# Kernel optimization log

Measured on AMD Instinct MI355X. Metric: run time of the kernel, lower is better.

## Reference

```python
import jax, jax.numpy as jnp
import numpy as np

EPS = 1e-8


def setup_inputs() -> dict:
    key = jax.random.key(0)
    ks = jax.random.split(key, 6)
    B, Cin, Cout, K, S, G = 8, 64, 64, 3, 512, 48
    fan_in = Cin * K * K * K
    bound_w = np.sqrt(6.0 / ((1 + 0.25 ** 2) * fan_in))  # kaiming_uniform a=0.25
    bound_b = 1.0 / np.sqrt(fan_in)
    bound_lin = 1.0 / np.sqrt(S)
    return {
        "x": jax.random.normal(ks[0], (B, Cin, G, G, G), jnp.float32),
        "style": jax.random.normal(ks[1], (B, S), jnp.float32),
        "weight": jax.random.uniform(ks[2], (Cout, Cin, K, K, K), jnp.float32, -bound_w, bound_w),
        "bias": jax.random.uniform(ks[3], (1, Cout, 1, 1, 1), jnp.float32, -bound_b, bound_b),
        "style_w": jax.random.uniform(ks[4], (Cin, S), jnp.float32, -bound_lin, bound_lin),
        "style_b": jax.random.uniform(ks[5], (Cin,), jnp.float32, -bound_lin, bound_lin),
    }


def reference(x, style, weight, bias, style_w, style_b):
    B, Cin = x.shape[0], x.shape[1]
    Cout, K = weight.shape[0], weight.shape[2]
    # style modulation scale per (sample, input channel)
    s = style @ style_w.T + style_b                      # [B, Cin]
    # modulate: per-sample weights [B, Cout, Cin, K, K, K]
    w = weight[None] * s[:, None, :, None, None, None]
    # demodulate: rsqrt of per-(sample, out-channel) variance
    var = jnp.sum(w * w, axis=(2, 3, 4, 5), keepdims=True)
    w = w * jax.lax.rsqrt(var + EPS)
    # grouped conv: merge batch into channels, groups = batch_size
    w = w.reshape(B * Cout, Cin, K, K, K)
    xg = x.reshape(1, B * Cin, *x.shape[2:])
    y = jax.lax.conv_general_dilated(
        xg, w,
        window_strides=(1, 1, 1),
        padding='VALID',
        dimension_numbers=('NCDHW', 'OIDHW', 'NCDHW'),
        feature_group_count=B,
    )
    y = y.reshape(B, Cout, *y.shape[2:])
    return y + bias
```

## Files before the change

### kernel.cpp

```cpp
#include <hip/hip_runtime.h>


typedef __bf16 bf16x8 __attribute__((ext_vector_type(8)));
typedef float  f32x4  __attribute__((ext_vector_type(4)));

static constexpr int   B_   = 8;
static constexpr int   S_   = 512;
static constexpr int   G_   = 48;
static constexpr int   O_   = 46;
static constexpr int   TAPS = 27;
static constexpr int   SPI  = G_ * G_ * G_;
static constexpr int   SPO  = O_ * O_ * O_;
static constexpr float EPSV = 1e-8f;

static constexpr size_t XT_OFF   = 0;
static constexpr size_t XT_BYTES = (size_t)B_ * SPI * 64 * 2;
static constexpr size_t WQ_OFF   = XT_OFF + XT_BYTES;
static constexpr size_t WQ_BYTES = (size_t)B_ * 2 * TAPS * 64 * 32 * 2;
static constexpr size_t S_OFF    = WQ_OFF + WQ_BYTES;
static constexpr size_t D_OFF    = S_OFF + 2048;

__device__ __forceinline__ unsigned short f2bf(float f) {
    unsigned int u = __float_as_uint(f);
    u = (u + 0x7fffu + ((u >> 16) & 1u)) >> 16;
    return (unsigned short)u;
}

__global__ void s_kernel(const float* __restrict__ style,
                         const float* __restrict__ style_w,
                         const float* __restrict__ style_b,
                         float* __restrict__ s_out)
{
    const int bg = blockIdx.x, b = bg >> 6, g = bg & 63, l = threadIdx.x;
    const float4* sp = (const float4*)(style + b * S_);
    const float4* wp = (const float4*)(style_w + g * S_);
    const float4 a0 = sp[l * 2], a1 = sp[l * 2 + 1];
    const float4 b0 = wp[l * 2], b1 = wp[l * 2 + 1];
    float acc = a0.x * b0.x + a0.y * b0.y + a0.z * b0.z + a0.w * b0.w
              + a1.x * b1.x + a1.y * b1.y + a1.z * b1.z + a1.w * b1.w;
#pragma unroll
    for (int m = 1; m <= 32; m <<= 1) acc += __shfl_xor(acc, m);
    if (l == 0) s_out[bg] = acc + style_b[g];
}

__global__ void d_kernel(const float* __restrict__ weight,
                         const float* __restrict__ s,
                         float* __restrict__ d_out)
{
    const int bc = blockIdx.x, b = bc >> 6, co = bc & 63, ci = threadIdx.x;
    const float sv = s[b * 64 + ci];
    const float* wp = weight + (co * 64 + ci) * TAPS;
    float v = 0.f;
#pragma unroll
    for (int i = 0; i < TAPS; ++i) { const float t = wp[i] * sv; v += t * t; }
#pragma unroll
    for (int m = 1; m <= 32; m <<= 1) v += __shfl_xor(v, m);
    if (ci == 0) d_out[bc] = rsqrtf(v + EPSV);
}

__global__ void wq_kernel(const float* __restrict__ weight,
                          const float* __restrict__ s,
                          const float* __restrict__ d,
                          unsigned short* __restrict__ wq)
{
    const int blk = blockIdx.x;
    const int b = blk / 27, tap = blk - b * 27;
    const int t = threadIdx.x;
#pragma unroll
    for (int it = 0; it < 2; ++it) {
        const int item = t + it * 256;
        const int kc = item >> 8;
        const int g  = (item >> 6) & 3;
        const int l  = item & 63;
        const int co = g * 16 + (l & 15);
        const int ci0 = kc * 32 + ((l >> 4) * 8);
        const float dd = d[b * 64 + co];
        unsigned int u[4];
#pragma unroll
        for (int k = 0; k < 4; ++k) {
            const int ci = ci0 + 2 * k;
            const float w0 = weight[(co * 64 + ci)     * TAPS + tap] * s[b * 64 + ci]     * dd;
            const float w1 = weight[(co * 64 + ci + 1) * TAPS + tap] * s[b * 64 + ci + 1] * dd;
            u[k] = (unsigned)f2bf(w0) | ((unsigned)f2bf(w1) << 16);
        }
        uint4 v; v.x = u[0]; v.y = u[1]; v.z = u[2]; v.w = u[3];
        *(uint4*)(wq + ((size_t)((b * 2 + kc) * 27 + tap)) * 2048 + (g * 64 + l) * 8) = v;
    }
}

__global__ void xT_kernel(const float* __restrict__ x,
                          unsigned short* __restrict__ xT)
{
    const int blk = blockIdx.x;
    const int b = blk / 1728;
    const int sp0 = (blk - b * 1728) * 64;
    const int t = threadIdx.x;
    __shared__ float tile[64][65];

    const int spl = t & 63;
    const int c4 = t >> 6;
#pragma unroll
    for (int p = 0; p < 16; ++p) {
        const int ci = c4 * 16 + p;
        tile[ci][spl] = x[((size_t)b * 64 + ci) * SPI + sp0 + spl];
    }
    __syncthreads();

    const int ci8 = (t & 7) * 8;
    const int spq = t >> 3;
#pragma unroll
    for (int p = 0; p < 2; ++p) {
        const int sp = spq + 32 * p;
        unsigned int u[4];
#pragma unroll
        for (int k = 0; k < 4; ++k) {
            const unsigned int lo = f2bf(tile[ci8 + 2 * k][sp]);
            const unsigned int hi = f2bf(tile[ci8 + 2 * k + 1][sp]);
            u[k] = lo | (hi << 16);
        }
        uint4 v; v.x = u[0]; v.y = u[1]; v.z = u[2]; v.w = u[3];
        *(uint4*)(xT + ((size_t)b * SPI + sp0 + sp) * 64 + ci8) = v;
    }
}

#define XST     80
#define XTILE_B (648 * 80)

__global__ __launch_bounds__(256, 3) void conv_kernel(
    const unsigned short* __restrict__ xT,
    const unsigned short* __restrict__ wq,
    const float* __restrict__ bias,
    float* __restrict__ out)
{
    __shared__ __align__(16) char xs[XTILE_B];

    const int t = threadIdx.x;
    const int p  = blockIdx.x;
    const int lg = (p & 7) * 432 + (p >> 3);
    const int xt = lg % 3;
    const int r0 = lg / 3;
    const int yt = r0 % 12;
    const int bz = r0 / 12;
    const int b  = bz / 12, zt = bz - b * 12;
    const int x0 = xt * 16;
    const int y0 = (yt < 11) ? yt * 4 : 42;
    const int z0 = (zt < 11) ? zt * 4 : 42;

    const unsigned short* const xb = xT + (size_t)b * (SPI * 64);
    const unsigned short* const wb = wq + (size_t)b * (2 * TAPS * 2048);

    const int w = t >> 6, l = t & 63, kg = l >> 4, l16 = l & 15;
    const int bbase = (w * 108 + l16) * XST + kg * 16;

    f32x4 acc[16];
#pragma unroll
    for (int i = 0; i < 16; ++i) acc[i] = (f32x4){0.f, 0.f, 0.f, 0.f};

#pragma unroll 1
    for (int kc = 0; kc < 2; ++kc) {
        const unsigned short* const wkc = wb + (size_t)kc * (TAPS * 2048);

        if (kc) __syncthreads();

        for (int i = t; i < 2592; i += 256) {
            const int sp = i >> 2, cg = i & 3;
            const int iz = sp / 108;
            const int r1 = sp - iz * 108;
            const int iy = r1 / 18;
            const int ix = r1 - iy * 18;
            int gx = x0 + ix; if (gx > 47) gx = 47;
            const uint4 v = *(const uint4*)(xb +
                ((((z0 + iz) * 48) + (y0 + iy)) * 48 + gx) * 64 + kc * 32 + cg * 8);
            *(uint4*)(xs + sp * XST + cg * 16) = v;
        }

        bf16x8 a[4];
#pragma unroll
        for (int g = 0; g < 4; ++g)
            a[g] = *(const bf16x8*)(wkc + g * 512 + l * 8);

        __syncthreads();

#pragma unroll 1
        for (int tap = 0; tap < TAPS; ++tap) {
            const int tnx = (tap + 1 < TAPS) ? tap + 1 : tap;
            bf16x8 an[4];
#pragma unroll
            for (int g = 0; g < 4; ++g)
                an[g] = *(const bf16x8*)(wkc + (size_t)tnx * 2048 + g * 512 + l * 8);

            const int kz = tap / 9;
            const int r2 = tap - kz * 9;
            const int ky = r2 / 3;
            const int kx = r2 - ky * 3;
            const int toff = ((kz * 6 + ky) * 18 + kx) * XST;

            bf16x8 b0 = *(const bf16x8*)(xs + toff + bbase);
            bf16x8 b1 = *(const bf16x8*)(xs + toff + bbase + 18 * XST);
            bf16x8 b2 = *(const bf16x8*)(xs + toff + bbase + 36 * XST);
            bf16x8 b3 = *(const bf16x8*)(xs + toff + bbase + 54 * XST);

            acc[0]  = __builtin_amdgcn_mfma_f32_16x16x32_bf16(a[0], b0, acc[0],  0, 0, 0);
            acc[1]  = __builtin_amdgcn_mfma_f32_16x16x32_bf16(a[0], b1, acc[1],  0, 0, 0);
            acc[2]  = __builtin_amdgcn_mfma_f32_16x16x32_bf16(a[0], b2, acc[2],  0, 0, 0);
            acc[3]  = __builtin_amdgcn_mfma_f32_16x16x32_bf16(a[0], b3, acc[3],  0, 0, 0);
            acc[4]  = __builtin_amdgcn_mfma_f32_16x16x32_bf16(a[1], b0, acc[4],  0, 0, 0);
            acc[5]  = __builtin_amdgcn_mfma_f32_16x16x32_bf16(a[1], b1, acc[5],  0, 0, 0);
            acc[6]  = __builtin_amdgcn_mfma_f32_16x16x32_bf16(a[1], b2, acc[6],  0, 0, 0);
            acc[7]  = __builtin_amdgcn_mfma_f32_16x16x32_bf16(a[1], b3, acc[7],  0, 0, 0);
            acc[8]  = __builtin_amdgcn_mfma_f32_16x16x32_bf16(a[2], b0, acc[8],  0, 0, 0);
            acc[9]  = __builtin_amdgcn_mfma_f32_16x16x32_bf16(a[2], b1, acc[9],  0, 0, 0);
            acc[10] = __builtin_amdgcn_mfma_f32_16x16x32_bf16(a[2], b2, acc[10], 0, 0, 0);
            acc[11] = __builtin_amdgcn_mfma_f32_16x16x32_bf16(a[2], b3, acc[11], 0, 0, 0);
            acc[12] = __builtin_amdgcn_mfma_f32_16x16x32_bf16(a[3], b0, acc[12], 0, 0, 0);
            acc[13] = __builtin_amdgcn_mfma_f32_16x16x32_bf16(a[3], b1, acc[13], 0, 0, 0);
            acc[14] = __builtin_amdgcn_mfma_f32_16x16x32_bf16(a[3], b2, acc[14], 0, 0, 0);
            acc[15] = __builtin_amdgcn_mfma_f32_16x16x32_bf16(a[3], b3, acc[15], 0, 0, 0);

#pragma unroll
            for (int g = 0; g < 4; ++g) a[g] = an[g];
        }
    }

    const size_t ob = (size_t)b * 64 * SPO;
    const int oz = z0 + w;
    const int ox = x0 + l16;
    const bool xok = (ox < O_);
    if (xok) {
#pragma unroll
        for (int g = 0; g < 4; ++g) {
#pragma unroll
            for (int nt = 0; nt < 4; ++nt) {
                const int oy = y0 + nt;
                const f32x4 v = acc[g * 4 + nt];
                const size_t so = (size_t)oz * 2116 + oy * 46 + ox;
#pragma unroll
                for (int r = 0; r < 4; ++r) {
                    const int co = g * 16 + kg * 4 + r;
                    out[ob + (size_t)co * SPO + so] = v[r] + bias[co];
                }
            }
        }
    }
}

extern "C" void kernel_launch(void* const* d_in, const int* in_sizes, int n_in,
                              void* d_out, int out_size, void* d_ws, size_t ws_size,
                              hipStream_t stream)
{
    const float* x       = (const float*)d_in[0];
    const float* style   = (const float*)d_in[1];
    const float* weight  = (const float*)d_in[2];
    const float* bias    = (const float*)d_in[3];
    const float* style_w = (const float*)d_in[4];
    const float* style_b = (const float*)d_in[5];
    float* out = (float*)d_out;

    char* ws = (char*)d_ws;
    unsigned short* xT  = (unsigned short*)(ws + XT_OFF);
    unsigned short* wqp = (unsigned short*)(ws + WQ_OFF);
    float* sbuf = (float*)(ws + S_OFF);
    float* dbuf = (float*)(ws + D_OFF);

    hipLaunchKernelGGL(s_kernel, dim3(512), dim3(64), 0, stream,
                       style, style_w, style_b, sbuf);
    hipLaunchKernelGGL(d_kernel, dim3(512), dim3(64), 0, stream,
                       weight, sbuf, dbuf);
    hipLaunchKernelGGL(wq_kernel, dim3(216), dim3(256), 0, stream,
                       weight, sbuf, dbuf, wqp);
    hipLaunchKernelGGL(xT_kernel, dim3(B_ * (SPI / 64)), dim3(256), 0, stream,
                       x, xT);
    hipLaunchKernelGGL(conv_kernel, dim3(3456), dim3(256), 0, stream,
                       xT, wqp, bias, out);
}
```

Baseline: 588.9 us.

## Prefetch second channel chunk into registers and remap warps to 2x8 output tiles

```diff
diff --git a/kernel.cpp b/kernel.cpp
--- a/kernel.cpp
+++ b/kernel.cpp
@@ -97,12 +97,16 @@
     const int t = threadIdx.x;
     __shared__ float tile[64][65];
 
-    const int spl = t & 63;
-    const int c4 = t >> 6;
-#pragma unroll
-    for (int p = 0; p < 16; ++p) {
-        const int ci = c4 * 16 + p;
-        tile[ci][spl] = x[((size_t)b * 64 + ci) * SPI + sp0 + spl];
+    const int cr = t >> 4;
+    const int s4 = (t & 15) * 4;
+#pragma unroll
+    for (int r = 0; r < 4; ++r) {
+        const int ci = r * 16 + cr;
+        const float4 v = *(const float4*)(x + ((size_t)b * 64 + ci) * SPI + sp0 + s4);
+        tile[ci][s4]     = v.x;
+        tile[ci][s4 + 1] = v.y;
+        tile[ci][s4 + 2] = v.z;
+        tile[ci][s4 + 3] = v.w;
     }
     __syncthreads();
 
@@ -150,93 +154,101 @@
     const unsigned short* const wb = wq + (size_t)b * (2 * TAPS * 2048);
 
     const int w = t >> 6, l = t & 63, kg = l >> 4, l16 = l & 15;
-    const int bbase = (w * 108 + l16) * XST + kg * 16;
+    const int ch = w & 1, zp = w >> 1;
+    const unsigned short* const wa = wb + ch * 1024 + l * 8;
+    const int bbase = (zp * 216 + l16) * XST + kg * 16;
+    constexpr int FOFF[8] = {0, 1440, 2880, 4320, 8640, 10080, 11520, 12960};
 
     f32x4 acc[16];
 #pragma unroll
     for (int i = 0; i < 16; ++i) acc[i] = (f32x4){0.f, 0.f, 0.f, 0.f};
 
+    auto x_src = [&](int i, int kc) -> const uint4* {
+        const int sp = i >> 2, cg = i & 3;
+        const int iz = sp / 108;
+        const int r1 = sp - iz * 108;
+        const int iy = r1 / 18;
+        const int ix = r1 - iy * 18;
+        int gx = x0 + ix; if (gx > 47) gx = 47;
+        return (const uint4*)(xb +
+            ((((z0 + iz) * 48) + (y0 + iy)) * 48 + gx) * 64 + kc * 32 + cg * 8);
+    };
+
+#pragma unroll
+    for (int j = 0; j < 10; ++j) {
+        const int i = t + j * 256;
+        const uint4 v = *x_src(i, 0);
+        *(uint4*)(xs + (i >> 2) * XST + (i & 3) * 16) = v;
+    }
+    if (t < 32) {
+        const int i = 2560 + t;
+        const uint4 v = *x_src(i, 0);
+        *(uint4*)(xs + (i >> 2) * XST + (i & 3) * 16) = v;
+    }
+
+    bf16x8 a0 = *(const bf16x8*)(wa);
+    bf16x8 a1 = *(const bf16x8*)(wa + 512);
+
+    __syncthreads();
+
+    uint4 pv[10];
+#pragma unroll
+    for (int j = 0; j < 10; ++j)
+        pv[j] = *x_src(t + j * 256, 1);
+
+    auto tap_body = [&](int kt, int ktn) {
+        const bf16x8 n0 = *(const bf16x8*)(wa + (size_t)ktn * 2048);
+        const bf16x8 n1 = *(const bf16x8*)(wa + (size_t)ktn * 2048 + 512);
+        const int tap = (kt >= 27) ? kt - 27 : kt;
+        const int kz = tap / 9;
+        const int r2 = tap - kz * 9;
+        const int ky = r2 / 3;
+        const int kx = r2 - ky * 3;
+        const int toff = (kz * 108 + ky * 18 + kx) * XST;
+#pragma unroll
+        for (int nf = 0; nf < 8; ++nf) {
+            const bf16x8 bv = *(const bf16x8*)(xs + toff + bbase + FOFF[nf]);
+            acc[nf]     = __builtin_amdgcn_mfma_f32_16x16x32_bf16(a0, bv, acc[nf],     0, 0, 0);
+            acc[8 + nf] = __builtin_amdgcn_mfma_f32_16x16x32_bf16(a1, bv, acc[8 + nf], 0, 0, 0);
+        }
+        a0 = n0; a1 = n1;
+    };
+
 #pragma unroll 1
-    for (int kc = 0; kc < 2; ++kc) {
-        const unsigned short* const wkc = wb + (size_t)kc * (TAPS * 2048);
-
-        if (kc) __syncthreads();
-
-        for (int i = t; i < 2592; i += 256) {
-            const int sp = i >> 2, cg = i & 3;
-            const int iz = sp / 108;
-            const int r1 = sp - iz * 108;
-            const int iy = r1 / 18;
-            const int ix = r1 - iy * 18;
-            int gx = x0 + ix; if (gx > 47) gx = 47;
-            const uint4 v = *(const uint4*)(xb +
-                ((((z0 + iz) * 48) + (y0 + iy)) * 48 + gx) * 64 + kc * 32 + cg * 8);
-            *(uint4*)(xs + sp * XST + cg * 16) = v;
-        }
-
-        bf16x8 a[4];
-#pragma unroll
-        for (int g = 0; g < 4; ++g)
-            a[g] = *(const bf16x8*)(wkc + g * 512 + l * 8);
-
-        __syncthreads();
+    for (int kt = 0; kt < 27; ++kt)
+        tap_body(kt, kt + 1);
+
+    __syncthreads();
+#pragma unroll
+    for (int j = 0; j < 10; ++j) {
+        const int i = t + j * 256;
+        *(uint4*)(xs + (i >> 2) * XST + (i & 3) * 16) = pv[j];
+    }
+    if (t < 32) {
+        const int i = 2560 + t;
+        const uint4 v = *x_src(i, 1);
+        *(uint4*)(xs + (i >> 2) * XST + (i & 3) * 16) = v;
+    }
+    __syncthreads();
 
 #pragma unroll 1
-        for (int tap = 0; tap < TAPS; ++tap) {
-            const int tnx = (tap + 1 < TAPS) ? tap + 1 : tap;
-            bf16x8 an[4];
-#pragma unroll
-            for (int g = 0; g < 4; ++g)
-                an[g] = *(const bf16x8*)(wkc + (size_t)tnx * 2048 + g * 512 + l * 8);
-
-            const int kz = tap / 9;
-            const int r2 = tap - kz * 9;
-            const int ky = r2 / 3;
-            const int kx = r2 - ky * 3;
-            const int toff = ((kz * 6 + ky) * 18 + kx) * XST;
-
-            bf16x8 b0 = *(const bf16x8*)(xs + toff + bbase);
-            bf16x8 b1 = *(const bf16x8*)(xs + toff + bbase + 18 * XST);
-            bf16x8 b2 = *(const bf16x8*)(xs + toff + bbase + 36 * XST);
-            bf16x8 b3 = *(const bf16x8*)(xs + toff + bbase + 54 * XST);
-
-            acc[0]  = __builtin_amdgcn_mfma_f32_16x16x32_bf16(a[0], b0, acc[0],  0, 0, 0);
-            acc[1]  = __builtin_amdgcn_mfma_f32_16x16x32_bf16(a[0], b1, acc[1],  0, 0, 0);
-            acc[2]  = __builtin_amdgcn_mfma_f32_16x16x32_bf16(a[0], b2, acc[2],  0, 0, 0);
-            acc[3]  = __builtin_amdgcn_mfma_f32_16x16x32_bf16(a[0], b3, acc[3],  0, 0, 0);
-            acc[4]  = __builtin_amdgcn_mfma_f32_16x16x32_bf16(a[1], b0, acc[4],  0, 0, 0);
-            acc[5]  = __builtin_amdgcn_mfma_f32_16x16x32_bf16(a[1], b1, acc[5],  0, 0, 0);
-            acc[6]  = __builtin_amdgcn_mfma_f32_16x16x32_bf16(a[1], b2, acc[6],  0, 0, 0);
-            acc[7]  = __builtin_amdgcn_mfma_f32_16x16x32_bf16(a[1], b3, acc[7],  0, 0, 0);
-            acc[8]  = __builtin_amdgcn_mfma_f32_16x16x32_bf16(a[2], b0, acc[8],  0, 0, 0);
-            acc[9]  = __builtin_amdgcn_mfma_f32_16x16x32_bf16(a[2], b1, acc[9],  0, 0, 0);
-            acc[10] = __builtin_amdgcn_mfma_f32_16x16x32_bf16(a[2], b2, acc[10], 0, 0, 0);
-            acc[11] = __builtin_amdgcn_mfma_f32_16x16x32_bf16(a[2], b3, acc[11], 0, 0, 0);
-            acc[12] = __builtin_amdgcn_mfma_f32_16x16x32_bf16(a[3], b0, acc[12], 0, 0, 0);
-            acc[13] = __builtin_amdgcn_mfma_f32_16x16x32_bf16(a[3], b1, acc[13], 0, 0, 0);
-            acc[14] = __builtin_amdgcn_mfma_f32_16x16x32_bf16(a[3], b2, acc[14], 0, 0, 0);
-            acc[15] = __builtin_amdgcn_mfma_f32_16x16x32_bf16(a[3], b3, acc[15], 0, 0, 0);
-
-#pragma unroll
-            for (int g = 0; g < 4; ++g) a[g] = an[g];
-        }
-    }
+    for (int kt = 27; kt < 54; ++kt)
+        tap_body(kt, (kt + 1 < 54) ? kt + 1 : 53);
 
     const size_t ob = (size_t)b * 64 * SPO;
-    const int oz = z0 + w;
     const int ox = x0 + l16;
-    const bool xok = (ox < O_);
-    if (xok) {
-#pragma unroll
-        for (int g = 0; g < 4; ++g) {
-#pragma unroll
-            for (int nt = 0; nt < 4; ++nt) {
-                const int oy = y0 + nt;
-                const f32x4 v = acc[g * 4 + nt];
+    if (ox < O_) {
+#pragma unroll
+        for (int cf = 0; cf < 2; ++cf) {
+#pragma unroll
+            for (int nf = 0; nf < 8; ++nf) {
+                const int oz = z0 + 2 * zp + (nf >> 2);
+                const int oy = y0 + (nf & 3);
+                const f32x4 v = acc[cf * 8 + nf];
                 const size_t so = (size_t)oz * 2116 + oy * 46 + ox;
 #pragma unroll
                 for (int r = 0; r < 4; ++r) {
-                    const int co = g * 16 + kg * 4 + r;
+                    const int co = ch * 32 + cf * 16 + kg * 4 + r;
                     out[ob + (size_t)co * SPO + so] = v[r] + bias[co];
                 }
             }
```

New measurement: 606.4 us. 3.0% more time.
